# Kernel tuning notes

Measured on AMD Instinct MI355X. Metric: run time of the kernel, lower is better.

Reference implementation:

```python
import jax, jax.numpy as jnp
import numpy as np

N = 384          # item_num (text regions)
TD = 768         # text hidden (bert-base)
VD = 768         # vision hidden (vit-base)
CD = TD + VD     # commu_dim = 1536
FF = 2048        # TransformerEncoderLayer default dim_feedforward
H = 4            # nhead
L = 2            # num_layers per encoder
EPS = 1e-5


def _enc_params(key, d, scale=0.02):
    ks = jax.random.split(key, 6)
    return dict(
        qkv_w=jax.random.normal(ks[0], (L, 3 * d, d), jnp.float32) * scale,
        qkv_b=jnp.zeros((L, 3 * d), jnp.float32),
        out_w=jax.random.normal(ks[1], (L, d, d), jnp.float32) * scale,
        out_b=jnp.zeros((L, d), jnp.float32),
        ln1_s=jnp.ones((L, d), jnp.float32),
        ln1_b=jnp.zeros((L, d), jnp.float32),
        ff1_w=jax.random.normal(ks[2], (L, FF, d), jnp.float32) * scale,
        ff1_b=jnp.zeros((L, FF), jnp.float32),
        ff2_w=jax.random.normal(ks[3], (L, d, FF), jnp.float32) * scale,
        ff2_b=jnp.zeros((L, d), jnp.float32),
        ln2_s=jnp.ones((L, d), jnp.float32),
        ln2_b=jnp.zeros((L, d), jnp.float32),
    )


def setup_inputs() -> dict:
    key = jax.random.key(0)
    k = jax.random.split(key, 6)
    inp = {
        'text_emb': jax.random.normal(k[0], (N, TD), jnp.float32),
        'vision_emb': jax.random.normal(k[1], (N, VD), jnp.float32),
        'gt_matrix': jax.random.randint(k[2], (N, N), 0, 2, jnp.int32),
    }
    for pref, kk, d in (('t_', k[3], TD), ('c_', k[4], CD)):
        for name, v in _enc_params(kk, d).items():
            inp[pref + name] = v
    inp['lin_w'] = jax.random.normal(k[5], (2, 2 * CD), jnp.float32) * 0.02
    inp['lin_b'] = jnp.zeros((2,), jnp.float32)
    return inp


def _ln(x, s, b):
    m = jnp.mean(x, -1, keepdims=True)
    v = jnp.mean((x - m) ** 2, -1, keepdims=True)
    return (x - m) * jax.lax.rsqrt(v + EPS) * s + b


def _encoder(x, qkv_w, qkv_b, out_w, out_b, ln1_s, ln1_b,
             ff1_w, ff1_b, ff2_w, ff2_b, ln2_s, ln2_b):
    # PyTorch post-norm TransformerEncoder, relu activation, eval mode (no dropout)
    d = x.shape[-1]
    hd = d // H
    for l in range(qkv_w.shape[0]):
        qkv = x @ qkv_w[l].T + qkv_b[l]
        q, kk, v = jnp.split(qkv, 3, axis=-1)
        q = q.reshape(-1, H, hd)
        kk = kk.reshape(-1, H, hd)
        v = v.reshape(-1, H, hd)
        scores = jnp.einsum('qhd,khd->hqk', q, kk) / jnp.sqrt(jnp.float32(hd))
        attn = jax.nn.softmax(scores, -1)
        o = jnp.einsum('hqk,khd->qhd', attn, v).reshape(-1, d)
        x = _ln(x + o @ out_w[l].T + out_b[l], ln1_s[l], ln1_b[l])
        h = jax.nn.relu(x @ ff1_w[l].T + ff1_b[l]) @ ff2_w[l].T + ff2_b[l]
        x = _ln(x + h, ln2_s[l], ln2_b[l])
    return x


def reference(text_emb, vision_emb, gt_matrix,
              t_qkv_w, t_qkv_b, t_out_w, t_out_b, t_ln1_s, t_ln1_b,
              t_ff1_w, t_ff1_b, t_ff2_w, t_ff2_b, t_ln2_s, t_ln2_b,
              c_qkv_w, c_qkv_b, c_out_w, c_out_b, c_ln1_s, c_ln1_b,
              c_ff1_w, c_ff1_b, c_ff2_w, c_ff2_b, c_ln2_s, c_ln2_b,
              lin_w, lin_b):
    te = _encoder(text_emb, t_qkv_w, t_qkv_b, t_out_w, t_out_b, t_ln1_s, t_ln1_b,
                  t_ff1_w, t_ff1_b, t_ff2_w, t_ff2_b, t_ln2_s, t_ln2_b)
    all_emb = jnp.concatenate([te, vision_emb], axis=1)  # [N, CD]
    all_emb = _encoder(all_emb, c_qkv_w, c_qkv_b, c_out_w, c_out_b, c_ln1_s, c_ln1_b,
                       c_ff1_w, c_ff1_b, c_ff2_w, c_ff2_b, c_ln2_s, c_ln2_b)
    # organize(): linear(cat(e_i, e_j)) decomposes exactly as e_i@Wa^T + e_j@Wb^T + b,
    # avoiding the O(N^2 * 2*CD) pair tensor while computing identical math.
    a = all_emb @ lin_w[:, :CD].T + lin_b      # [N, 2]
    c = all_emb @ lin_w[:, CD:].T              # [N, 2]
    logits = a[:, None, :] + c[None, :, :]     # [N, N, 2]
    probs = jax.nn.softmax(logits, -1)         # self.activate(self.linear(...))
    # classificaiton_loss: sum_i CrossEntropyLoss(probs[i], gt[i])  (CE takes probs as logits)
    ls = jax.nn.log_softmax(probs, -1)
    cell = -jnp.take_along_axis(ls, gt_matrix[..., None].astype(jnp.int32), axis=-1)[..., 0]
    cls_loss = jnp.sum(jnp.mean(cell, axis=1))
    # enter_exit_loss over first N-1 items
    link = probs[:, :, 1]
    ee_loss = jnp.sum(jnp.abs(link.sum(1)[:-1] + link.sum(0)[:-1] - 1.0))
    return probs, cls_loss, ee_loss
```

## Files before the change

### kernel.cpp

```cpp
#include <hip/hip_runtime.h>
#include <hip/hip_bf16.h>
#include <math.h>

#define NTOK 384
#define HEADS 4

typedef __attribute__((ext_vector_type(8))) short bf16x8;
typedef __attribute__((ext_vector_type(4))) float f32x4;

__device__ __forceinline__ unsigned short f2b(float f) {
    union { float f; unsigned int u; } v; v.f = f;
    unsigned int r = (v.u + 0x7fff + ((v.u >> 16) & 1)) >> 16;
    return (unsigned short)r;
}

__device__ __forceinline__ void g2l16(const void* g, void* l) {
    __builtin_amdgcn_global_load_lds(
        (const __attribute__((address_space(1))) unsigned int*)g,
        (__attribute__((address_space(3))) unsigned int*)l, 16, 0, 0);
}

__device__ __forceinline__ void stage64(
    const unsigned short* __restrict__ g, int row0, int k0, int ld,
    char* region, int wid, int lane)
{
    int c = wid * 64 + lane;
    int row = c >> 2, p = c & 3;
    int kc = (p - (row >> 1)) & 3;
    g2l16(g + (long)(row0 + row) * ld + k0 + kc * 8,
          region + (wid * 64) * 16);
}

__device__ __forceinline__ void stage_tile(
    const unsigned short* __restrict__ A, const unsigned short* __restrict__ B,
    int row0, int col0, int k0, int lda, int ldb,
    char* buf, int wid, int lane)
{
    stage64(A, row0, k0,      lda, buf,         wid, lane);
    stage64(A, row0, k0 + 32, lda, buf +  4096, wid, lane);
    stage64(B, col0, k0,      ldb, buf +  8192, wid, lane);
    stage64(B, col0, k0 + 32, ldb, buf + 12288, wid, lane);
    __builtin_amdgcn_sched_barrier(0);
}

__global__ __launch_bounds__(256, 3) void gemm64(
    const unsigned short* __restrict__ A, const unsigned short* __restrict__ B,
    const float* __restrict__ bias, void* __restrict__ Cv,
    int K, int lda, int ldb, int ldc,
    long sA, long sB, long sC, int relu, int out_bf16,
    unsigned short* __restrict__ vt, int dv2)
{
    __shared__ char smem[3][16384];
    A += (long)blockIdx.z * sA;
    B += (long)blockIdx.z * sB;
    const int t = threadIdx.x, lane = t & 63, wid = t >> 6;
    const int wm = wid >> 1, wn = wid & 1;
    const int r16 = lane & 15, quad = lane >> 4;
    const int row0 = blockIdx.y * 64, col0 = blockIdx.x * 64;

    f32x4 acc[2][2] = {};
    const int NT = K >> 6;

    stage_tile(A, B, row0, col0, 0, lda, ldb, smem[0], wid, lane);
    if (NT > 1)
        stage_tile(A, B, row0, col0, 64, lda, ldb, smem[1], wid, lane);

    int cur = 0, sb = 2;
    for (int kt = 0; kt < NT; ++kt) {
        if (kt + 1 < NT) asm volatile("s_waitcnt vmcnt(4)" ::: "memory");
        else             asm volatile("s_waitcnt vmcnt(0) lgkmcnt(0)" ::: "memory");
        __builtin_amdgcn_s_barrier();
        if (kt + 2 < NT) {
            stage_tile(A, B, row0, col0, (kt + 2) * 64, lda, ldb,
                       smem[sb], wid, lane);
            sb = (sb == 2) ? 0 : sb + 1;
        }
        const char* cb = smem[cur];
        cur = (cur == 2) ? 0 : cur + 1;
        #pragma unroll
        for (int h = 0; h < 2; ++h) {
            bf16x8 af[2], bfv[2];
            #pragma unroll
            for (int rt = 0; rt < 2; ++rt) {
                int row = wm * 32 + rt * 16 + r16;
                int p = (quad + (row >> 1)) & 3;
                af[rt] = *reinterpret_cast<const bf16x8*>(
                    cb + h * 4096 + row * 64 + p * 16);
            }
            #pragma unroll
            for (int ct = 0; ct < 2; ++ct) {
                int col = wn * 32 + ct * 16 + r16;
                int p = (quad + (col >> 1)) & 3;
                bfv[ct] = *reinterpret_cast<const bf16x8*>(
                    cb + 8192 + h * 4096 + col * 64 + p * 16);
            }
            #pragma unroll
            for (int rt = 0; rt < 2; ++rt)
                #pragma unroll
                for (int ct = 0; ct < 2; ++ct)
                    acc[rt][ct] = __builtin_amdgcn_mfma_f32_16x16x32_bf16(
                        af[rt], bfv[ct], acc[rt][ct], 0, 0, 0);
        }
    }

    float* Cf = (float*)Cv;
    unsigned short* Cb = (unsigned short*)Cv;
    const long zoff = (long)blockIdx.z * sC;
    const int vwrite = (vt != nullptr) && (col0 >= dv2);
    #pragma unroll
    for (int rt = 0; rt < 2; ++rt) {
        #pragma unroll
        for (int ct = 0; ct < 2; ++ct) {
            f32x4 v = acc[rt][ct];
            int col = col0 + wn * 32 + ct * 16 + r16;
            float bi = bias ? bias[col] : 0.f;
            #pragma unroll
            for (int i = 0; i < 4; ++i) {
                v[i] += bi;
                if (relu) v[i] = fmaxf(v[i], 0.f);
            }
            int rbase = row0 + wm * 32 + rt * 16 + quad * 4;
            if (vwrite) {
                ushort4 p;
                p.x = f2b(v[0]); p.y = f2b(v[1]); p.z = f2b(v[2]); p.w = f2b(v[3]);
                *reinterpret_cast<ushort4*>(vt + (long)(col - dv2) * NTOK + rbase) = p;
            } else if (out_bf16) {
                #pragma unroll
                for (int i = 0; i < 4; ++i)
                    Cb[zoff + (long)(rbase + i) * ldc + col] = f2b(v[i]);
            } else {
                #pragma unroll
                for (int i = 0; i < 4; ++i)
                    Cf[zoff + (long)(rbase + i) * ldc + col] = v[i];
            }
        }
    }
}

#define WO0 0u
#define WO1 3538944u
#define WO2 4718592u
#define WO3 7864320u
#define WO4 11010048u
#define WO5 25165824u
#define WO6 29884416u
#define WO7 36175872u
#define WTOT 42467328u

__global__ __launch_bounds__(256) void convert_weights(
    const float* __restrict__ s0, const float* __restrict__ s1,
    const float* __restrict__ s2, const float* __restrict__ s3,
    const float* __restrict__ s4, const float* __restrict__ s5,
    const float* __restrict__ s6, const float* __restrict__ s7,
    unsigned short* __restrict__ dst)
{
    unsigned int e = (blockIdx.x * 256u + threadIdx.x) * 8u;
    if (e >= WTOT) return;
    const float* src; unsigned int local;
    if      (e < WO1) { src = s0; local = e - WO0; }
    else if (e < WO2) { src = s1; local = e - WO1; }
    else if (e < WO3) { src = s2; local = e - WO2; }
    else if (e < WO4) { src = s3; local = e - WO3; }
    else if (e < WO5) { src = s4; local = e - WO4; }
    else if (e < WO6) { src = s5; local = e - WO5; }
    else if (e < WO7) { src = s6; local = e - WO6; }
    else              { src = s7; local = e - WO7; }
    float4 v0 = *reinterpret_cast<const float4*>(src + local);
    float4 v1 = *reinterpret_cast<const float4*>(src + local + 4);
    uint4 o;
    o.x = (unsigned)f2b(v0.x) | ((unsigned)f2b(v0.y) << 16);
    o.y = (unsigned)f2b(v0.z) | ((unsigned)f2b(v0.w) << 16);
    o.z = (unsigned)f2b(v1.x) | ((unsigned)f2b(v1.y) << 16);
    o.w = (unsigned)f2b(v1.z) | ((unsigned)f2b(v1.w) << 16);
    *reinterpret_cast<uint4*>(dst + e) = o;
}

__global__ __launch_bounds__(64) void softmax_rows(
    const float* __restrict__ S, unsigned short* __restrict__ P, float scale)
{
    const float* p = S + (long)blockIdx.x * NTOK;
    unsigned short* q = P + (long)blockIdx.x * NTOK;
    const int t = threadIdx.x;
    float vals[6];
    float vmax = -1e30f;
    #pragma unroll
    for (int i = 0; i < 6; ++i) {
        vals[i] = p[t + i * 64] * scale;
        vmax = fmaxf(vmax, vals[i]);
    }
    for (int off = 32; off; off >>= 1) vmax = fmaxf(vmax, __shfl_down(vmax, off));
    vmax = __shfl(vmax, 0);
    float sum = 0.f;
    #pragma unroll
    for (int i = 0; i < 6; ++i) { vals[i] = __expf(vals[i] - vmax); sum += vals[i]; }
    for (int off = 32; off; off >>= 1) sum += __shfl_down(sum, off);
    sum = __shfl(sum, 0);
    float inv = 1.f / sum;
    #pragma unroll
    for (int i = 0; i < 6; ++i) q[t + i * 64] = f2b(vals[i] * inv);
}

__global__ __launch_bounds__(256) void add_ln(
    float* __restrict__ x, unsigned short* __restrict__ xb,
    const float* __restrict__ y,
    const float* __restrict__ s, const float* __restrict__ b, int d)
{
    float* xr = x + (long)blockIdx.x * d;
    unsigned short* xbr = xb + (long)blockIdx.x * d;
    const float* yr = y + (long)blockIdx.x * d;
    const int t = threadIdx.x;
    float s1 = 0.f, s2 = 0.f;
    for (int i = t; i < d; i += 256) {
        float v = xr[i] + yr[i];
        s1 += v; s2 += v * v;
    }
    for (int off = 32; off; off >>= 1) { s1 += __shfl_down(s1, off); s2 += __shfl_down(s2, off); }
    __shared__ float r1[4], r2[4];
    int w = t >> 6;
    if ((t & 63) == 0) { r1[w] = s1; r2[w] = s2; }
    __syncthreads();
    if (t == 0) {
        float a = 0.f, c = 0.f;
        for (int i = 0; i < 4; ++i) { a += r1[i]; c += r2[i]; }
        r1[0] = a; r2[0] = c;
    }
    __syncthreads();
    float mean = r1[0] / d;
    float var = r2[0] / d - mean * mean;
    float rstd = rsqrtf(var + 1e-5f);
    for (int i = t; i < d; i += 256) {
        float v = (xr[i] + yr[i] - mean) * rstd * s[i] + b[i];
        xr[i] = v;
        xbr[i] = f2b(v);
    }
}

__global__ void initx_k(const float* __restrict__ src, float* __restrict__ dst,
                        unsigned short* __restrict__ dstb, int n)
{
    int i = blockIdx.x * blockDim.x + threadIdx.x;
    if (i < n) { float v = src[i]; dst[i] = v; dstb[i] = f2b(v); }
}

__global__ void concat_k(const float* __restrict__ te, const float* __restrict__ ve,
                         float* __restrict__ all, unsigned short* __restrict__ allb)
{
    int i = blockIdx.x * blockDim.x + threadIdx.x;
    if (i >= NTOK * 1536) return;
    int r = i / 1536, c = i % 1536;
    float v = (c < 768) ? te[r * 768 + c] : ve[r * 768 + (c - 768)];
    all[i] = v;
    allb[i] = f2b(v);
}

__global__ __launch_bounds__(256) void head_ac(
    const float* __restrict__ all, const float* __restrict__ lin_w,
    const float* __restrict__ lin_b, float* __restrict__ a, float* __restrict__ c)
{
    const int i = blockIdx.x, t = threadIdx.x;
    const float* xr = all + (long)i * 1536;
    float s0 = 0.f, s1 = 0.f, s2 = 0.f, s3 = 0.f;
    for (int e = t; e < 1536; e += 256) {
        float v = xr[e];
        s0 += v * lin_w[e];
        s1 += v * lin_w[3072 + e];
        s2 += v * lin_w[1536 + e];
        s3 += v * lin_w[4608 + e];
    }
    for (int off = 32; off; off >>= 1) {
        s0 += __shfl_down(s0, off); s1 += __shfl_down(s1, off);
        s2 += __shfl_down(s2, off); s3 += __shfl_down(s3, off);
    }
    __shared__ float r[4][4];
    int w = t >> 6;
    if ((t & 63) == 0) { r[0][w] = s0; r[1][w] = s1; r[2][w] = s2; r[3][w] = s3; }
    __syncthreads();
    if (t == 0) {
        float t0 = 0.f, t1 = 0.f, t2 = 0.f, t3 = 0.f;
        for (int k = 0; k < 4; ++k) { t0 += r[0][k]; t1 += r[1][k]; t2 += r[2][k]; t3 += r[3][k]; }
        a[i * 2 + 0] = t0 + lin_b[0];
        a[i * 2 + 1] = t1 + lin_b[1];
        c[i * 2 + 0] = t2;
        c[i * 2 + 1] = t3;
    }
}

__global__ __launch_bounds__(384) void head_probs(
    const float* __restrict__ a, const float* __restrict__ c,
    const int* __restrict__ gt, float* __restrict__ probs,
    float* __restrict__ rowsum, float* __restrict__ rowcell)
{
    const int i = blockIdx.x, j = threadIdx.x;
    float l0 = a[i * 2 + 0] + c[j * 2 + 0];
    float l1 = a[i * 2 + 1] + c[j * 2 + 1];
    float m = fmaxf(l0, l1);
    float e0 = __expf(l0 - m), e1 = __expf(l1 - m);
    float inv = 1.f / (e0 + e1);
    float p0 = e0 * inv, p1 = e1 * inv;
    long base = ((long)i * NTOK + j) * 2;
    probs[base] = p0;
    probs[base + 1] = p1;
    float m2 = fmaxf(p0, p1);
    float z = m2 + __logf(__expf(p0 - m2) + __expf(p1 - m2));
    int g = gt[i * NTOK + j];
    float cell = z - (g ? p1 : p0);
    float cs = cell, ps = p1;
    for (int off = 32; off; off >>= 1) { cs += __shfl_down(cs, off); ps += __shfl_down(ps, off); }
    __shared__ float rc[6], rs[6];
    int w = j >> 6;
    if ((j & 63) == 0) { rc[w] = cs; rs[w] = ps; }
    __syncthreads();
    if (j == 0) {
        float csum = 0.f, psum = 0.f;
        for (int k = 0; k < 6; ++k) { csum += rc[k]; psum += rs[k]; }
        rowcell[i] = csum * (1.f / NTOK);
        rowsum[i] = psum;
    }
}

__global__ __launch_bounds__(64) void colsum_k(const float* __restrict__ probs,
                                               float* __restrict__ colsum)
{
    const int j = blockIdx.x, t = threadIdx.x;
    float s = 0.f;
    for (int i = t; i < NTOK; i += 64)
        s += probs[((long)i * NTOK + j) * 2 + 1];
    for (int off = 32; off; off >>= 1) s += __shfl_down(s, off);
    if (t == 0) colsum[j] = s;
}

__global__ __launch_bounds__(384) void finalize_k(
    const float* __restrict__ rowcell, const float* __restrict__ rowsum,
    const float* __restrict__ colsum, float* __restrict__ out)
{
    const int t = threadIdx.x;
    float cls = rowcell[t];
    float ee = (t < NTOK - 1) ? fabsf(rowsum[t] + colsum[t] - 1.f) : 0.f;
    for (int off = 32; off; off >>= 1) { cls += __shfl_down(cls, off); ee += __shfl_down(ee, off); }
    __shared__ float rc[6], re[6];
    int w = t >> 6;
    if ((t & 63) == 0) { rc[w] = cls; re[w] = ee; }
    __syncthreads();
    if (t == 0) {
        float a = 0.f, b = 0.f;
        for (int k = 0; k < 6; ++k) { a += rc[k]; b += re[k]; }
        out[NTOK * NTOK * 2 + 0] = a;
        out[NTOK * NTOK * 2 + 1] = b;
    }
}

static void run_encoder(float* x, unsigned short* xb, int d,
                        const unsigned short* wq, const unsigned short* wo,
                        const unsigned short* w1, const unsigned short* w2,
                        const float* qkv_b, const float* out_b,
                        const float* ln1_s, const float* ln1_b,
                        const float* ff1_b, const float* ff2_b,
                        const float* ln2_s, const float* ln2_b,
                        unsigned short* qkvb, float* sc, unsigned short* attnb,
                        unsigned short* vtb, unsigned short* ob,
                        unsigned short* t1b, float* t2,
                        hipStream_t stream)
{
    const int dq = 3 * d;
    const int hd = d / HEADS;
    const float scale = 1.0f / sqrtf((float)hd);
    for (int l = 0; l < 2; ++l) {
        gemm64<<<dim3(dq / 64, 6), 256, 0, stream>>>(
            xb, wq + (long)l * dq * d, qkv_b + l * dq, qkvb,
            d, d, d, dq, 0, 0, 0, 0, 1, vtb, 2 * d);
        gemm64<<<dim3(6, 6, HEADS), 256, 0, stream>>>(
            qkvb, qkvb + d, nullptr, sc,
            hd, dq, dq, NTOK, (long)hd, (long)hd, (long)NTOK * NTOK,
            0, 0, nullptr, 0);
        softmax_rows<<<HEADS * NTOK, 64, 0, stream>>>(sc, attnb, scale);
        gemm64<<<dim3(hd / 64, 6, HEADS), 256, 0, stream>>>(
            attnb, vtb, nullptr, ob,
            NTOK, NTOK, NTOK, d, (long)NTOK * NTOK, (long)hd * NTOK, (long)hd,
            0, 1, nullptr, 0);
        gemm64<<<dim3(d / 64, 6), 256, 0, stream>>>(
            ob, wo + (long)l * d * d, out_b + l * d, t2,
            d, d, d, d, 0, 0, 0, 0, 0, nullptr, 0);
        add_ln<<<NTOK, 256, 0, stream>>>(x, xb, t2, ln1_s + l * d, ln1_b + l * d, d);
        gemm64<<<dim3(2048 / 64, 6), 256, 0, stream>>>(
            xb, w1 + (long)l * 2048 * d, ff1_b + l * 2048, t1b,
            d, d, d, 2048, 0, 0, 0, 1, 1, nullptr, 0);
        gemm64<<<dim3(d / 64, 6), 256, 0, stream>>>(
            t1b, w2 + (long)l * d * 2048, ff2_b + l * d, t2,
            2048, 2048, 2048, d, 0, 0, 0, 0, 0, nullptr, 0);
        add_ln<<<NTOK, 256, 0, stream>>>(x, xb, t2, ln2_s + l * d, ln2_b + l * d, d);
    }
}

extern "C" void kernel_launch(void* const* d_in, const int* in_sizes, int n_in,
                              void* d_out, int out_size, void* d_ws, size_t ws_size,
                              hipStream_t stream)
{
    const float* text_emb   = (const float*)d_in[0];
    const float* vision_emb = (const float*)d_in[1];
    const int*   gt         = (const int*)  d_in[2];
    const float* t_qkv_w = (const float*)d_in[3];
    const float* t_qkv_b = (const float*)d_in[4];
    const float* t_out_w = (const float*)d_in[5];
    const float* t_out_b = (const float*)d_in[6];
    const float* t_ln1_s = (const float*)d_in[7];
    const float* t_ln1_b = (const float*)d_in[8];
    const float* t_ff1_w = (const float*)d_in[9];
    const float* t_ff1_b = (const float*)d_in[10];
    const float* t_ff2_w = (const float*)d_in[11];
    const float* t_ff2_b = (const float*)d_in[12];
    const float* t_ln2_s = (const float*)d_in[13];
    const float* t_ln2_b = (const float*)d_in[14];
    const float* c_qkv_w = (const float*)d_in[15];
    const float* c_qkv_b = (const float*)d_in[16];
    const float* c_out_w = (const float*)d_in[17];
    const float* c_out_b = (const float*)d_in[18];
    const float* c_ln1_s = (const float*)d_in[19];
    const float* c_ln1_b = (const float*)d_in[20];
    const float* c_ff1_w = (const float*)d_in[21];
    const float* c_ff1_b = (const float*)d_in[22];
    const float* c_ff2_w = (const float*)d_in[23];
    const float* c_ff2_b = (const float*)d_in[24];
    const float* c_ln2_s = (const float*)d_in[25];
    const float* c_ln2_b = (const float*)d_in[26];
    const float* lin_w   = (const float*)d_in[27];
    const float* lin_b   = (const float*)d_in[28];
    float* out = (float*)d_out;

    float* ws = (float*)d_ws;
    float* xt      = ws;
    float* all     = xt + 294912;
    float* t2      = all + 589824;
    float* sc      = t2 + 589824;
    float* abuf    = sc + 589824;
    float* cbuf    = abuf + 768;
    float* rowsum  = cbuf + 768;
    float* rowcell = rowsum + 384;
    float* colsum  = rowcell + 384;
    unsigned short* ub = (unsigned short*)(ws + 2067072);
    unsigned short* xtb   = ub;
    unsigned short* allb  = xtb + 294912;
    unsigned short* qkvb  = allb + 589824;
    unsigned short* attnb = qkvb + 1769472;
    unsigned short* vtb   = attnb + 589824;
    unsigned short* ob    = vtb + 589824;
    unsigned short* t1b   = ob + 589824;
    unsigned short* wb    = t1b + 786432;

    convert_weights<<<(WTOT / 8 + 255) / 256, 256, 0, stream>>>(
        t_qkv_w, t_out_w, t_ff1_w, t_ff2_w,
        c_qkv_w, c_out_w, c_ff1_w, c_ff2_w, wb);

    initx_k<<<(294912 + 255) / 256, 256, 0, stream>>>(text_emb, xt, xtb, 294912);
    run_encoder(xt, xtb, 768,
                wb + WO0, wb + WO1, wb + WO2, wb + WO3,
                t_qkv_b, t_out_b, t_ln1_s, t_ln1_b,
                t_ff1_b, t_ff2_b, t_ln2_s, t_ln2_b,
                qkvb, sc, attnb, vtb, ob, t1b, t2, stream);

    concat_k<<<(589824 + 255) / 256, 256, 0, stream>>>(xt, vision_emb, all, allb);
    run_encoder(all, allb, 1536,
                wb + WO4, wb + WO5, wb + WO6, wb + WO7,
                c_qkv_b, c_out_b, c_ln1_s, c_ln1_b,
                c_ff1_b, c_ff2_b, c_ln2_s, c_ln2_b,
                qkvb, sc, attnb, vtb, ob, t1b, t2, stream);

    head_ac<<<NTOK, 256, 0, stream>>>(all, lin_w, lin_b, abuf, cbuf);
    head_probs<<<NTOK, 384, 0, stream>>>(abuf, cbuf, gt, out, rowsum, rowcell);
    colsum_k<<<NTOK, 64, 0, stream>>>(out, colsum);
    finalize_k<<<1, 384, 0, stream>>>(rowcell, rowsum, colsum, out);
}
```

Baseline: 501.8 us.

## Overlap combined-encoder weight conversion with text-encoder GEMMs and deepen pipeline

The combined encoder's fp32->bf16 weight conversion no longer runs as one upfront kernel. It is split into chunks that extra blocks appended to each text-encoder GEMM grid process, so the conversion runs alongside the small, underfilled GEMMs. The GEMM also moves from triple to quadruple LDS buffering with a three-tile prefetch depth, and launch bounds drop from 3 to 2 blocks per CU. The chunking only fully covers the weights if the text encoder has enough GEMM launches. Larger LDS and lower occupancy could slow GEMMs that were latency-bound.

```diff
diff --git a/kernel.cpp b/kernel.cpp
--- a/kernel.cpp
+++ b/kernel.cpp
@@ -43,14 +43,43 @@
     __builtin_amdgcn_sched_barrier(0);
 }
 
-__global__ __launch_bounds__(256, 3) void gemm64(
+__global__ __launch_bounds__(256, 2) void gemm64(
     const unsigned short* __restrict__ A, const unsigned short* __restrict__ B,
     const float* __restrict__ bias, void* __restrict__ Cv,
     int K, int lda, int ldb, int ldc,
     long sA, long sB, long sC, int relu, int out_bf16,
-    unsigned short* __restrict__ vt, int dv2)
-{
-    __shared__ char smem[3][16384];
+    unsigned short* __restrict__ vt, int dv2,
+    int gx, const float* __restrict__ cw, unsigned short* __restrict__ cd,
+    long cn)
+{
+    __shared__ char smem[4][16384];
+
+    if (blockIdx.x >= (unsigned)gx) {
+        const int tt = threadIdx.x;
+        const long nxb = (long)gridDim.x - gx;
+        const long wbid = (blockIdx.x - gx) +
+                          nxb * (blockIdx.y + (long)gridDim.y * blockIdx.z);
+        const long nwb = nxb * gridDim.y * gridDim.z;
+        for (long e = (wbid * 256 + tt) * 16; e < cn; e += nwb * 4096) {
+            float4 v0 = *reinterpret_cast<const float4*>(cw + e);
+            float4 v1 = *reinterpret_cast<const float4*>(cw + e + 4);
+            float4 v2 = *reinterpret_cast<const float4*>(cw + e + 8);
+            float4 v3 = *reinterpret_cast<const float4*>(cw + e + 12);
+            uint4 o0, o1;
+            o0.x = (unsigned)f2b(v0.x) | ((unsigned)f2b(v0.y) << 16);
+            o0.y = (unsigned)f2b(v0.z) | ((unsigned)f2b(v0.w) << 16);
+            o0.z = (unsigned)f2b(v1.x) | ((unsigned)f2b(v1.y) << 16);
+            o0.w = (unsigned)f2b(v1.z) | ((unsigned)f2b(v1.w) << 16);
+            o1.x = (unsigned)f2b(v2.x) | ((unsigned)f2b(v2.y) << 16);
+            o1.y = (unsigned)f2b(v2.z) | ((unsigned)f2b(v2.w) << 16);
+            o1.z = (unsigned)f2b(v3.x) | ((unsigned)f2b(v3.y) << 16);
+            o1.w = (unsigned)f2b(v3.z) | ((unsigned)f2b(v3.w) << 16);
+            *reinterpret_cast<uint4*>(cd + e) = o0;
+            *reinterpret_cast<uint4*>(cd + e + 8) = o1;
+        }
+        return;
+    }
+
     A += (long)blockIdx.z * sA;
     B += (long)blockIdx.z * sB;
     const int t = threadIdx.x, lane = t & 63, wid = t >> 6;
@@ -62,21 +91,19 @@
     const int NT = K >> 6;
 
     stage_tile(A, B, row0, col0, 0, lda, ldb, smem[0], wid, lane);
-    if (NT > 1)
-        stage_tile(A, B, row0, col0, 64, lda, ldb, smem[1], wid, lane);
-
-    int cur = 0, sb = 2;
+    if (NT > 1) stage_tile(A, B, row0, col0,  64, lda, ldb, smem[1], wid, lane);
+    if (NT > 2) stage_tile(A, B, row0, col0, 128, lda, ldb, smem[2], wid, lane);
+
     for (int kt = 0; kt < NT; ++kt) {
-        if (kt + 1 < NT) asm volatile("s_waitcnt vmcnt(4)" ::: "memory");
-        else             asm volatile("s_waitcnt vmcnt(0) lgkmcnt(0)" ::: "memory");
+        const int rem = NT - 1 - kt;
+        if (rem >= 2)      asm volatile("s_waitcnt vmcnt(8)" ::: "memory");
+        else if (rem == 1) asm volatile("s_waitcnt vmcnt(4)" ::: "memory");
+        else               asm volatile("s_waitcnt vmcnt(0) lgkmcnt(0)" ::: "memory");
         __builtin_amdgcn_s_barrier();
-        if (kt + 2 < NT) {
-            stage_tile(A, B, row0, col0, (kt + 2) * 64, lda, ldb,
-                       smem[sb], wid, lane);
-            sb = (sb == 2) ? 0 : sb + 1;
-        }
-        const char* cb = smem[cur];
-        cur = (cur == 2) ? 0 : cur + 1;
+        if (kt + 3 < NT)
+            stage_tile(A, B, row0, col0, (kt + 3) * 64, lda, ldb,
+                       smem[(kt + 3) & 3], wid, lane);
+        const char* cb = smem[kt & 3];
         #pragma unroll
         for (int h = 0; h < 2; ++h) {
             bf16x8 af[2], bfv[2];
@@ -146,25 +173,20 @@
 #define WO6 29884416u
 #define WO7 36175872u
 #define WTOT 42467328u
-
-__global__ __launch_bounds__(256) void convert_weights(
+#define TTOT 11010048u
+
+__global__ __launch_bounds__(256) void convert_text(
     const float* __restrict__ s0, const float* __restrict__ s1,
     const float* __restrict__ s2, const float* __restrict__ s3,
-    const float* __restrict__ s4, const float* __restrict__ s5,
-    const float* __restrict__ s6, const float* __restrict__ s7,
     unsigned short* __restrict__ dst)
 {
     unsigned int e = (blockIdx.x * 256u + threadIdx.x) * 8u;
-    if (e >= WTOT) return;
+    if (e >= TTOT) return;
     const float* src; unsigned int local;
     if      (e < WO1) { src = s0; local = e - WO0; }
     else if (e < WO2) { src = s1; local = e - WO1; }
     else if (e < WO3) { src = s2; local = e - WO2; }
-    else if (e < WO4) { src = s3; local = e - WO3; }
-    else if (e < WO5) { src = s4; local = e - WO4; }
-    else if (e < WO6) { src = s5; local = e - WO5; }
-    else if (e < WO7) { src = s6; local = e - WO6; }
-    else              { src = s7; local = e - WO7; }
+    else              { src = s3; local = e - WO3; }
     float4 v0 = *reinterpret_cast<const float4*>(src + local);
     float4 v1 = *reinterpret_cast<const float4*>(src + local + 4);
     uint4 o;
@@ -349,6 +371,20 @@
     }
 }
 
+struct CvtCur {
+    const float* srcs[4]; unsigned short* dsts[4]; long lens[4];
+    int ti; long off;
+    void next(long want, const float** s, unsigned short** d, long* n) {
+        if (ti >= 4) { *s = nullptr; *d = nullptr; *n = 0; return; }
+        long rem = lens[ti] - off;
+        long take = want < rem ? want : rem;
+        *s = srcs[ti] + off; *d = dsts[ti] + off; *n = take;
+        off += take;
+        if (off == lens[ti]) { ti++; off = 0; }
+    }
+};
+#define CVT_W 3200000L
+
 static void run_encoder(float* x, unsigned short* xb, int d,
                         const unsigned short* wq, const unsigned short* wo,
                         const unsigned short* w1, const unsigned short* w2,
@@ -359,36 +395,63 @@
                         unsigned short* qkvb, float* sc, unsigned short* attnb,
                         unsigned short* vtb, unsigned short* ob,
                         unsigned short* t1b, float* t2,
-                        hipStream_t stream)
+                        CvtCur* cvt, hipStream_t stream)
 {
     const int dq = 3 * d;
     const int hd = d / HEADS;
     const float scale = 1.0f / sqrtf((float)hd);
+    const float* cs; unsigned short* cds; long cl;
+    #define CHUNK(EXYZ) \
+        cs = nullptr; cds = nullptr; cl = 0; int ex = 0; \
+        if (cvt) { cvt->next(CVT_W, &cs, &cds, &cl); if (cl > 0) ex = (EXYZ); }
     for (int l = 0; l < 2; ++l) {
-        gemm64<<<dim3(dq / 64, 6), 256, 0, stream>>>(
-            xb, wq + (long)l * dq * d, qkv_b + l * dq, qkvb,
-            d, d, d, dq, 0, 0, 0, 0, 1, vtb, 2 * d);
-        gemm64<<<dim3(6, 6, HEADS), 256, 0, stream>>>(
-            qkvb, qkvb + d, nullptr, sc,
-            hd, dq, dq, NTOK, (long)hd, (long)hd, (long)NTOK * NTOK,
-            0, 0, nullptr, 0);
+        {
+            CHUNK(40);
+            gemm64<<<dim3(dq / 64 + ex, 6), 256, 0, stream>>>(
+                xb, wq + (long)l * dq * d, qkv_b + l * dq, qkvb,
+                d, d, d, dq, 0, 0, 0, 0, 1, vtb, 2 * d,
+                dq / 64, cs, cds, cl);
+        }
+        {
+            CHUNK(10);
+            gemm64<<<dim3(6 + ex, 6, HEADS), 256, 0, stream>>>(
+                qkvb, qkvb + d, nullptr, sc,
+                hd, dq, dq, NTOK, (long)hd, (long)hd, (long)NTOK * NTOK,
+                0, 0, nullptr, 0, 6, cs, cds, cl);
+        }
         softmax_rows<<<HEADS * NTOK, 64, 0, stream>>>(sc, attnb, scale);
-        gemm64<<<dim3(hd / 64, 6, HEADS), 256, 0, stream>>>(
-            attnb, vtb, nullptr, ob,
-            NTOK, NTOK, NTOK, d, (long)NTOK * NTOK, (long)hd * NTOK, (long)hd,
-            0, 1, nullptr, 0);
-        gemm64<<<dim3(d / 64, 6), 256, 0, stream>>>(
-            ob, wo + (long)l * d * d, out_b + l * d, t2,
-            d, d, d, d, 0, 0, 0, 0, 0, nullptr, 0);
+        {
+            CHUNK(10);
+            gemm64<<<dim3(hd / 64 + ex, 6, HEADS), 256, 0, stream>>>(
+                attnb, vtb, nullptr, ob,
+                NTOK, NTOK, NTOK, d, (long)NTOK * NTOK, (long)hd * NTOK, (long)hd,
+                0, 1, nullptr, 0, hd / 64, cs, cds, cl);
+        }
+        {
+            CHUNK(40);
+            gemm64<<<dim3(d / 64 + ex, 6), 256, 0, stream>>>(
+                ob, wo + (long)l * d * d, out_b + l * d, t2,
+                d, d, d, d, 0, 0, 0, 0, 0, nullptr, 0,
+                d / 64, cs, cds, cl);
+        }
         add_ln<<<NTOK, 256, 0, stream>>>(x, xb, t2, ln1_s + l * d, ln1_b + l * d, d);
-        gemm64<<<dim3(2048 / 64, 6), 256, 0, stream>>>(
-            xb, w1 + (long)l * 2048 * d, ff1_b + l * 2048, t1b,
-            d, d, d, 2048, 0, 0, 0, 1, 1, nullptr, 0);
-        gemm64<<<dim3(d / 64, 6), 256, 0, stream>>>(
-            t1b, w2 + (long)l * d * 2048, ff2_b + l * d, t2,
-            2048, 2048, 2048, d, 0, 0, 0, 0, 0, nullptr, 0);
+        {
+            CHUNK(40);
+            gemm64<<<dim3(2048 / 64 + ex, 6), 256, 0, stream>>>(
+                xb, w1 + (long)l * 2048 * d, ff1_b + l * 2048, t1b,
+                d, d, d, 2048, 0, 0, 0, 1, 1, nullptr, 0,
+                2048 / 64, cs, cds, cl);
+        }
+        {
+            CHUNK(40);
+            gemm64<<<dim3(d / 64 + ex, 6), 256, 0, stream>>>(
+                t1b, w2 + (long)l * d * 2048, ff2_b + l * d, t2,
+                2048, 2048, 2048, d, 0, 0, 0, 0, 0, nullptr, 0,
+                d / 64, cs, cds, cl);
+        }
         add_ln<<<NTOK, 256, 0, stream>>>(x, xb, t2, ln2_s + l * d, ln2_b + l * d, d);
     }
+    #undef CHUNK
 }
 
 extern "C" void kernel_launch(void* const* d_in, const int* in_sizes, int n_in,
@@ -446,23 +509,29 @@
     unsigned short* t1b   = ob + 589824;
     unsigned short* wb    = t1b + 786432;
 
-    convert_weights<<<(WTOT / 8 + 255) / 256, 256, 0, stream>>>(
-        t_qkv_w, t_out_w, t_ff1_w, t_ff2_w,
-        c_qkv_w, c_out_w, c_ff1_w, c_ff2_w, wb);
+    convert_text<<<(TTOT / 8 + 255) / 256, 256, 0, stream>>>(
+        t_qkv_w, t_out_w, t_ff1_w, t_ff2_w, wb);
+
+    CvtCur cvt;
+    cvt.srcs[0] = c_qkv_w; cvt.dsts[0] = wb + WO4; cvt.lens[0] = 14155776;
+    cvt.srcs[1] = c_out_w; cvt.dsts[1] = wb + WO5; cvt.lens[1] = 4718592;
+    cvt.srcs[2] = c_ff1_w; cvt.dsts[2] = wb + WO6; cvt.lens[2] = 6291456;
+    cvt.srcs[3] = c_ff2_w; cvt.dsts[3] = wb + WO7; cvt.lens[3] = 6291456;
+    cvt.ti = 0; cvt.off = 0;
 
     initx_k<<<(294912 + 255) / 256, 256, 0, stream>>>(text_emb, xt, xtb, 294912);
     run_encoder(xt, xtb, 768,
                 wb + WO0, wb + WO1, wb + WO2, wb + WO3,
                 t_qkv_b, t_out_b, t_ln1_s, t_ln1_b,
                 t_ff1_b, t_ff2_b, t_ln2_s, t_ln2_b,
-                qkvb, sc, attnb, vtb, ob, t1b, t2, stream);
+                qkvb, sc, attnb, vtb, ob, t1b, t2, &cvt, stream);
 
     concat_k<<<(589824 + 255) / 256, 256, 0, stream>>>(xt, vision_emb, all, allb);
     run_encoder(all, allb, 1536,
                 wb + WO4, wb + WO5, wb + WO6, wb + WO7,
                 c_qkv_b, c_out_b, c_ln1_s, c_ln1_b,
                 c_ff1_b, c_ff2_b, c_ln2_s, c_ln2_b,
-                qkvb, sc, attnb, vtb, ob, t1b, t2, stream);
+                qkvb, sc, attnb, vtb, ob, t1b, t2, nullptr, stream);
 
     head_ac<<<NTOK, 256, 0, stream>>>(all, lin_w, lin_b, abuf, cbuf);
     head_probs<<<NTOK, 384, 0, stream>>>(abuf, cbuf, gt, out, rowsum, rowcell);
```

New measurement: 512.6 us. 1.02x slower.

## Split-K the out-proj and FF2 GEMMs, reducing partials in fused add+LayerNorm

Applied to the files above, without the earlier changes.

The out-projection and FF2 GEMMs now use split-K over the grid z dimension (2-3 and 4 partitions), writing fp32 partial tiles that add_ln sums together with the bias and residual before normalizing. This is meant to fix under-occupancy, since the old grids launched only 72-144 blocks on a GPU with many CUs. add_ln also caches its values in registers, and convert_weights processes 16 elements per thread. The cost is extra partial-buffer memory traffic and a larger workspace.

```diff
diff --git a/kernel.cpp b/kernel.cpp
--- a/kernel.cpp
+++ b/kernel.cpp
@@ -154,7 +154,7 @@
     const float* __restrict__ s6, const float* __restrict__ s7,
     unsigned short* __restrict__ dst)
 {
-    unsigned int e = (blockIdx.x * 256u + threadIdx.x) * 8u;
+    unsigned int e = (blockIdx.x * 256u + threadIdx.x) * 16u;
     if (e >= WTOT) return;
     const float* src; unsigned int local;
     if      (e < WO1) { src = s0; local = e - WO0; }
@@ -167,12 +167,19 @@
     else              { src = s7; local = e - WO7; }
     float4 v0 = *reinterpret_cast<const float4*>(src + local);
     float4 v1 = *reinterpret_cast<const float4*>(src + local + 4);
-    uint4 o;
-    o.x = (unsigned)f2b(v0.x) | ((unsigned)f2b(v0.y) << 16);
-    o.y = (unsigned)f2b(v0.z) | ((unsigned)f2b(v0.w) << 16);
-    o.z = (unsigned)f2b(v1.x) | ((unsigned)f2b(v1.y) << 16);
-    o.w = (unsigned)f2b(v1.z) | ((unsigned)f2b(v1.w) << 16);
-    *reinterpret_cast<uint4*>(dst + e) = o;
+    float4 v2 = *reinterpret_cast<const float4*>(src + local + 8);
+    float4 v3 = *reinterpret_cast<const float4*>(src + local + 12);
+    uint4 o0, o1;
+    o0.x = (unsigned)f2b(v0.x) | ((unsigned)f2b(v0.y) << 16);
+    o0.y = (unsigned)f2b(v0.z) | ((unsigned)f2b(v0.w) << 16);
+    o0.z = (unsigned)f2b(v1.x) | ((unsigned)f2b(v1.y) << 16);
+    o0.w = (unsigned)f2b(v1.z) | ((unsigned)f2b(v1.w) << 16);
+    o1.x = (unsigned)f2b(v2.x) | ((unsigned)f2b(v2.y) << 16);
+    o1.y = (unsigned)f2b(v2.z) | ((unsigned)f2b(v2.w) << 16);
+    o1.z = (unsigned)f2b(v3.x) | ((unsigned)f2b(v3.y) << 16);
+    o1.w = (unsigned)f2b(v3.z) | ((unsigned)f2b(v3.w) << 16);
+    *reinterpret_cast<uint4*>(dst + e) = o0;
+    *reinterpret_cast<uint4*>(dst + e + 8) = o1;
 }
 
 __global__ __launch_bounds__(64) void softmax_rows(
@@ -202,17 +209,25 @@
 
 __global__ __launch_bounds__(256) void add_ln(
     float* __restrict__ x, unsigned short* __restrict__ xb,
-    const float* __restrict__ y,
+    const float* __restrict__ y, long ps, int np,
+    const float* __restrict__ gb,
     const float* __restrict__ s, const float* __restrict__ b, int d)
 {
     float* xr = x + (long)blockIdx.x * d;
     unsigned short* xbr = xb + (long)blockIdx.x * d;
     const float* yr = y + (long)blockIdx.x * d;
     const int t = threadIdx.x;
+    float vv[6];
     float s1 = 0.f, s2 = 0.f;
-    for (int i = t; i < d; i += 256) {
-        float v = xr[i] + yr[i];
-        s1 += v; s2 += v * v;
+    #pragma unroll
+    for (int j = 0; j < 6; ++j) {
+        int i = t + j * 256;
+        if (j * 256 < d) {
+            float v = xr[i] + gb[i];
+            for (int p = 0; p < np; ++p) v += yr[i + p * ps];
+            vv[j] = v;
+            s1 += v; s2 += v * v;
+        }
     }
     for (int off = 32; off; off >>= 1) { s1 += __shfl_down(s1, off); s2 += __shfl_down(s2, off); }
     __shared__ float r1[4], r2[4];
@@ -228,10 +243,14 @@
     float mean = r1[0] / d;
     float var = r2[0] / d - mean * mean;
     float rstd = rsqrtf(var + 1e-5f);
-    for (int i = t; i < d; i += 256) {
-        float v = (xr[i] + yr[i] - mean) * rstd * s[i] + b[i];
-        xr[i] = v;
-        xbr[i] = f2b(v);
+    #pragma unroll
+    for (int j = 0; j < 6; ++j) {
+        int i = t + j * 256;
+        if (j * 256 < d) {
+            float v = (vv[j] - mean) * rstd * s[i] + b[i];
+            xr[i] = v;
+            xbr[i] = f2b(v);
+        }
     }
 }
 
@@ -364,6 +383,10 @@
     const int dq = 3 * d;
     const int hd = d / HEADS;
     const float scale = 1.0f / sqrtf((float)hd);
+    const int np_out = (d == 768) ? 2 : 3;
+    const int ks_out = d / np_out;
+    const int np_ff2 = 4, ks_ff2 = 512;
+    const long psC = (long)NTOK * d;
     for (int l = 0; l < 2; ++l) {
         gemm64<<<dim3(dq / 64, 6), 256, 0, stream>>>(
             xb, wq + (long)l * dq * d, qkv_b + l * dq, qkvb,
@@ -377,17 +400,19 @@
             attnb, vtb, nullptr, ob,
             NTOK, NTOK, NTOK, d, (long)NTOK * NTOK, (long)hd * NTOK, (long)hd,
             0, 1, nullptr, 0);
-        gemm64<<<dim3(d / 64, 6), 256, 0, stream>>>(
-            ob, wo + (long)l * d * d, out_b + l * d, t2,
-            d, d, d, d, 0, 0, 0, 0, 0, nullptr, 0);
-        add_ln<<<NTOK, 256, 0, stream>>>(x, xb, t2, ln1_s + l * d, ln1_b + l * d, d);
+        gemm64<<<dim3(d / 64, 6, np_out), 256, 0, stream>>>(
+            ob, wo + (long)l * d * d, nullptr, t2,
+            ks_out, d, d, d, (long)ks_out, (long)ks_out, psC, 0, 0, nullptr, 0);
+        add_ln<<<NTOK, 256, 0, stream>>>(x, xb, t2, psC, np_out,
+                                         out_b + l * d, ln1_s + l * d, ln1_b + l * d, d);
         gemm64<<<dim3(2048 / 64, 6), 256, 0, stream>>>(
             xb, w1 + (long)l * 2048 * d, ff1_b + l * 2048, t1b,
             d, d, d, 2048, 0, 0, 0, 1, 1, nullptr, 0);
-        gemm64<<<dim3(d / 64, 6), 256, 0, stream>>>(
-            t1b, w2 + (long)l * d * 2048, ff2_b + l * d, t2,
-            2048, 2048, 2048, d, 0, 0, 0, 0, 0, nullptr, 0);
-        add_ln<<<NTOK, 256, 0, stream>>>(x, xb, t2, ln2_s + l * d, ln2_b + l * d, d);
+        gemm64<<<dim3(d / 64, 6, np_ff2), 256, 0, stream>>>(
+            t1b, w2 + (long)l * d * 2048, nullptr, t2,
+            ks_ff2, 2048, 2048, d, (long)ks_ff2, (long)ks_ff2, psC, 0, 0, nullptr, 0);
+        add_ln<<<NTOK, 256, 0, stream>>>(x, xb, t2, psC, np_ff2,
+                                         ff2_b + l * d, ln2_s + l * d, ln2_b + l * d, d);
     }
 }
 
@@ -430,13 +455,13 @@
     float* xt      = ws;
     float* all     = xt + 294912;
     float* t2      = all + 589824;
-    float* sc      = t2 + 589824;
+    float* sc      = t2 + 2359296;
     float* abuf    = sc + 589824;
     float* cbuf    = abuf + 768;
     float* rowsum  = cbuf + 768;
     float* rowcell = rowsum + 384;
     float* colsum  = rowcell + 384;
-    unsigned short* ub = (unsigned short*)(ws + 2067072);
+    unsigned short* ub = (unsigned short*)(ws + 3836544);
     unsigned short* xtb   = ub;
     unsigned short* allb  = xtb + 294912;
     unsigned short* qkvb  = allb + 589824;
@@ -446,7 +471,7 @@
     unsigned short* t1b   = ob + 589824;
     unsigned short* wb    = t1b + 786432;
 
-    convert_weights<<<(WTOT / 8 + 255) / 256, 256, 0, stream>>>(
+    convert_weights<<<(WTOT / 16 + 255) / 256, 256, 0, stream>>>(
         t_qkv_w, t_out_w, t_ff1_w, t_ff2_w,
         c_qkv_w, c_out_w, c_ff1_w, c_ff2_w, wb);
 
```

Measured after the change: 514.4 us. 1.03x slower.
